# Kernel tuning notes

Hardware: AMD Instinct MI355X
Metric: run time of the kernel (lower is better)

The kernel has to match this reference:

```python
import jax, jax.numpy as jnp
import numpy as np

H, W, D = 200, 200, 16          # voxel grid dims
GRID = 0.4                       # voxel size (m)
MULT = 3.0                       # scale_multiplier (3-sigma radius)
PC_MIN = np.array([-40.0, -40.0, -1.0], dtype=np.float32)
B, N, M, C = 1, 16384, 4096, 18  # batch, query points, gaussians, semantic classes


def setup_inputs() -> dict:
    key = jax.random.key(0)
    ks = jax.random.split(key, 6)
    extent = jnp.array([H, W, D], dtype=jnp.float32) * GRID
    pc_min = jnp.asarray(PC_MIN)
    # points / means strictly inside the grid so int-voxel asserts hold
    pts = pc_min + jax.random.uniform(ks[0], (B, N, 3), dtype=jnp.float32) * (extent - 1e-3)
    means3D = pc_min + jax.random.uniform(ks[1], (B, M, 3), dtype=jnp.float32) * (extent - 1e-3)
    opacities = jax.random.uniform(ks[2], (B, M), dtype=jnp.float32, minval=0.1, maxval=1.0)
    semantics = jax.random.normal(ks[3], (B, M, C), dtype=jnp.float32)
    # scales chosen so ceil(max_scale*3/0.4) >= 1 (radii assert)
    scales = jax.random.uniform(ks[4], (B, M, 3), dtype=jnp.float32, minval=0.15, maxval=0.6)
    # SPD covariance per Gaussian: diag(scales^2) + small PSD perturbation
    Bm = 0.05 * jax.random.normal(ks[5], (B, M, 3, 3), dtype=jnp.float32)
    cov3D = jnp.eye(3, dtype=jnp.float32) * (scales ** 2)[..., :, None] + Bm @ jnp.swapaxes(Bm, -1, -2)
    return {"pts": pts, "means3D": means3D, "opacities": opacities,
            "semantics": semantics, "scales": scales, "cov3D": cov3D}


def _aggregate(pts_i, means_i, op_i, sem_i, sc_i, cov_i):
    # pts_i [N,3], means_i [M,3], op_i [M], sem_i [M,C], sc_i [M,3], cov_i [M,3,3]
    pc_min = jnp.asarray(PC_MIN)
    pint = jnp.floor((pts_i - pc_min) / GRID).astype(jnp.int32)    # [N,3] voxel of each point
    mint = jnp.floor((means_i - pc_min) / GRID).astype(jnp.int32)  # [M,3] voxel of each gaussian
    radii = jnp.ceil(jnp.max(sc_i, axis=-1) * MULT / GRID).astype(jnp.int32)  # [M] voxel radius
    A = jnp.linalg.inv(cov_i)                                       # [M,3,3] conic (inverse cov)
    Am = jnp.einsum('gij,gj->gi', A, means_i)                       # [M,3]
    mAm = jnp.einsum('gi,gi->g', means_i, Am)                       # [M]
    # Mahalanobis q[n,g] = (p-m)^T A (p-m) = p^T A p - 2 p^T A m + m^T A m, via [N,9]x[9,M] GEMM
    pp = (pts_i[:, :, None] * pts_i[:, None, :]).reshape(-1, 9)     # [N,9]
    pAp = pp @ A.reshape(-1, 9).T                                   # [N,M]
    q = pAp - 2.0 * (pts_i @ Am.T) + mAm[None, :]                   # [N,M]
    # gaussian contributes to a point iff the point's voxel lies in the gaussian's radius box
    mask = jnp.all(jnp.abs(pint[:, None, :] - mint[None, :, :]) <= radii[None, :, None], axis=-1)
    w = jnp.where(mask, jnp.exp(-0.5 * q) * op_i[None, :], 0.0)     # [N,M]
    return w @ sem_i                                                # [N,C] logits


def reference(pts, means3D, opacities, semantics, scales, cov3D):
    return jax.vmap(_aggregate)(pts, means3D, opacities, semantics, scales, cov3D)
```

## Files before the change

### kernel.cpp

```cpp
#include <hip/hip_runtime.h>

namespace {
constexpr float GRIDSZ = 0.4f;
constexpr float PCX = -40.0f, PCY = -40.0f, PCZ = -1.0f;
constexpr int CCH = 18;
constexpr int CELLS_X = 25;
constexpr int NCELLS = CELLS_X * CELLS_X;
constexpr int VMAX = 199;
constexpr int PCAP = 128;
constexpr int GCAP = 128;
constexpr int SEMW = 20;
}

__global__ __launch_bounds__(256) void prep_kernel(
    const float* __restrict__ pts, const float* __restrict__ means,
    const float* __restrict__ opac, const float* __restrict__ scales,
    const float* __restrict__ cov,
    unsigned* __restrict__ ppack, float4* __restrict__ ppos,
    unsigned* __restrict__ gcb, int4* __restrict__ gbox,
    float4* __restrict__ gpay, int N, int M) {
  int id = blockIdx.x * 256 + threadIdx.x;
  if (id < M) {
    int g = id;
    float mx = means[(size_t)g * 3 + 0], my = means[(size_t)g * 3 + 1], mz = means[(size_t)g * 3 + 2];
    const float* c = cov + (size_t)g * 9;
    float c00 = c[0], c01 = c[1], c02 = c[2], c11 = c[4], c12 = c[5], c22 = c[8];
    float M00 = c11 * c22 - c12 * c12;
    float M01 = c02 * c12 - c01 * c22;
    float M02 = c01 * c12 - c02 * c11;
    float inv = 1.0f / (c00 * M00 + c01 * M01 + c02 * M02);
    int mvx = (int)floorf((mx - PCX) / GRIDSZ);
    int mvy = (int)floorf((my - PCY) / GRIDSZ);
    int mvz = (int)floorf((mz - PCZ) / GRIDSZ);
    float smax = fmaxf(scales[(size_t)g * 3 + 0],
                 fmaxf(scales[(size_t)g * 3 + 1], scales[(size_t)g * 3 + 2]));
    int r = (int)ceilf(smax * 3.0f / GRIDSZ);
    gbox[g] = make_int4(mvx - r, mvy - r, mvz - r, 2 * r);
    int cx0 = max(mvx - r, 0) >> 3, cx1 = min(mvx + r, VMAX) >> 3;
    int cy0 = max(mvy - r, 0) >> 3, cy1 = min(mvy + r, VMAX) >> 3;
    gcb[g] = (unsigned)cx0 | ((unsigned)cx1 << 8) | ((unsigned)cy0 << 16) | ((unsigned)cy1 << 24);
    gpay[(size_t)g * 3 + 0] = make_float4(mx, my, mz, opac[g]);
    gpay[(size_t)g * 3 + 1] = make_float4(M00 * inv, M01 * inv, M02 * inv,
                                          (c00 * c22 - c02 * c02) * inv);
    gpay[(size_t)g * 3 + 2] = make_float4((c01 * c02 - c00 * c12) * inv,
                                          (c00 * c11 - c01 * c01) * inv, 0.f, 0.f);
  } else if (id < M + N) {
    int p = id - M;
    float px = pts[(size_t)p * 3 + 0], py = pts[(size_t)p * 3 + 1], pz = pts[(size_t)p * 3 + 2];
    int pvx = (int)floorf((px - PCX) / GRIDSZ);
    int pvy = (int)floorf((py - PCY) / GRIDSZ);
    int pvz = (int)floorf((pz - PCZ) / GRIDSZ);
    unsigned cell = (unsigned)((pvx >> 3) + CELLS_X * (pvy >> 3));
    ppack[p] = cell | ((unsigned)pvx << 10) | ((unsigned)pvy << 18) | ((unsigned)pvz << 26);
    ppos[p] = make_float4(px, py, pz, __int_as_float(p));
  }
}

__global__ __launch_bounds__(256) void agg_kernel(
    const unsigned* __restrict__ ppack, const float4* __restrict__ ppos,
    const unsigned* __restrict__ gcb, const int4* __restrict__ gbox,
    const float4* __restrict__ gpay, const float* __restrict__ sem,
    float* __restrict__ out, int N, int M) {
  __shared__ int pcnt_s, gcnt_s;
  __shared__ unsigned lvox[PCAP];
  __shared__ int lpi[PCAP];
  __shared__ float4 lpts[PCAP];
  __shared__ int graw[GCAP];
  __shared__ int gsrt[GCAP];
  __shared__ int4 lbox[GCAP];
  __shared__ float4 lpay[GCAP * 3];
  __shared__ float lsem[GCAP * SEMW];
  __shared__ float buf[3][64][CCH + 1];

  const int tid = threadIdx.x, lane = tid & 63, wave = tid >> 6;
  const unsigned cell = blockIdx.x;
  const int cx = (int)(cell % CELLS_X), cy = (int)(cell / CELLS_X);

  if (tid == 0) { pcnt_s = 0; gcnt_s = 0; }
  __syncthreads();

  {
    const uint4* pp4 = reinterpret_cast<const uint4*>(ppack);
    const int n4 = N >> 2;
    for (int i4 = tid; i4 < n4; i4 += 256) {
      uint4 v = pp4[i4];
      unsigned pk[4] = {v.x, v.y, v.z, v.w};
#pragma unroll
      for (int k = 0; k < 4; ++k) {
        if ((pk[k] & 1023u) == cell) {
          int s = atomicAdd(&pcnt_s, 1);
          if (s < PCAP) { lvox[s] = pk[k]; lpi[s] = i4 * 4 + k; }
        }
      }
    }
    for (int i = (n4 << 2) + tid; i < N; i += 256) {
      unsigned pk = ppack[i];
      if ((pk & 1023u) == cell) {
        int s = atomicAdd(&pcnt_s, 1);
        if (s < PCAP) { lvox[s] = pk; lpi[s] = i; }
      }
    }
  }
  {
    const uint4* gb4 = reinterpret_cast<const uint4*>(gcb);
    const int m4 = M >> 2;
    for (int i4 = tid; i4 < m4; i4 += 256) {
      uint4 v = gb4[i4];
      unsigned gk[4] = {v.x, v.y, v.z, v.w};
#pragma unroll
      for (int k = 0; k < 4; ++k) {
        unsigned pk = gk[k];
        bool hit = (cx >= (int)(pk & 255u)) & (cx <= (int)((pk >> 8) & 255u)) &
                   (cy >= (int)((pk >> 16) & 255u)) & (cy <= (int)(pk >> 24));
        if (hit) {
          int s = atomicAdd(&gcnt_s, 1);
          if (s < GCAP) graw[s] = i4 * 4 + k;
        }
      }
    }
    for (int g = (m4 << 2) + tid; g < M; g += 256) {
      unsigned pk = gcb[g];
      bool hit = (cx >= (int)(pk & 255u)) & (cx <= (int)((pk >> 8) & 255u)) &
                 (cy >= (int)((pk >> 16) & 255u)) & (cy <= (int)(pk >> 24));
      if (hit) {
        int s = atomicAdd(&gcnt_s, 1);
        if (s < GCAP) graw[s] = g;
      }
    }
  }
  __syncthreads();
  const int P = min(pcnt_s, PCAP);
  const int K = min(gcnt_s, GCAP);

  if (tid < K) {
    int v = graw[tid], rank = 0;
    for (int j = 0; j < K; ++j) rank += (graw[j] < v);
    gsrt[rank] = v;
  }
  __syncthreads();

  if (tid < P) lpts[tid] = ppos[lpi[tid]];
  for (int j = tid; j < K; j += 256) lbox[j] = gbox[gsrt[j]];
  for (int idx = tid; idx < K * 3; idx += 256) {
    int j = idx / 3, k = idx - j * 3;
    lpay[idx] = gpay[(size_t)gsrt[j] * 3 + k];
  }
  for (int idx = tid; idx < K * CCH; idx += 256) {
    int j = idx / CCH, c2 = idx - j * CCH;
    lsem[j * SEMW + c2] = sem[(size_t)gsrt[j] * CCH + c2];
  }
  __syncthreads();

  const int kq = (K + 3) >> 2;
  const int j0 = wave * kq, j1 = min(K, j0 + kq);

  for (int pb = 0; pb < P; pb += 64) {
    const bool vp = (pb + lane) < P;
    const float4 pt = lpts[vp ? pb + lane : 0];
    const unsigned pk = vp ? lvox[pb + lane] : 0u;
    int pvx = (int)((pk >> 10) & 255u);
    int pvy = (int)((pk >> 18) & 255u);
    int pvz = (int)(pk >> 26);
    if (!vp) pvx = -100000;

    float acc[CCH];
#pragma unroll
    for (int c = 0; c < CCH; ++c) acc[c] = 0.f;

    for (int j = j0; j < j1; ++j) {
      int4 bx = lbox[j];
      bool m = ((unsigned)(pvx - bx.x) <= (unsigned)bx.w) &
               ((unsigned)(pvy - bx.y) <= (unsigned)bx.w) &
               ((unsigned)(pvz - bx.z) <= (unsigned)bx.w);
      if (__any(m)) {
        float4 q0 = lpay[j * 3 + 0];
        float4 q1 = lpay[j * 3 + 1];
        float4 q2 = lpay[j * 3 + 2];
        float dx = pt.x - q0.x, dy = pt.y - q0.y, dz = pt.z - q0.z;
        float t0 = q1.x * dx + q1.y * dy + q1.z * dz;
        float t1 = q1.y * dx + q1.w * dy + q2.x * dz;
        float t2 = q1.z * dx + q2.x * dy + q2.y * dz;
        float qq = dx * t0 + dy * t1 + dz * t2;
        float w = m ? __expf(-0.5f * qq) * q0.w : 0.f;
        const float4* s4 = reinterpret_cast<const float4*>(&lsem[j * SEMW]);
        float4 sa = s4[0], sb = s4[1], sc = s4[2], sd = s4[3];
        float2 se = *reinterpret_cast<const float2*>(&lsem[j * SEMW + 16]);
        acc[0]  = fmaf(w, sa.x, acc[0]);  acc[1]  = fmaf(w, sa.y, acc[1]);
        acc[2]  = fmaf(w, sa.z, acc[2]);  acc[3]  = fmaf(w, sa.w, acc[3]);
        acc[4]  = fmaf(w, sb.x, acc[4]);  acc[5]  = fmaf(w, sb.y, acc[5]);
        acc[6]  = fmaf(w, sb.z, acc[6]);  acc[7]  = fmaf(w, sb.w, acc[7]);
        acc[8]  = fmaf(w, sc.x, acc[8]);  acc[9]  = fmaf(w, sc.y, acc[9]);
        acc[10] = fmaf(w, sc.z, acc[10]); acc[11] = fmaf(w, sc.w, acc[11]);
        acc[12] = fmaf(w, sd.x, acc[12]); acc[13] = fmaf(w, sd.y, acc[13]);
        acc[14] = fmaf(w, sd.z, acc[14]); acc[15] = fmaf(w, sd.w, acc[15]);
        acc[16] = fmaf(w, se.x, acc[16]); acc[17] = fmaf(w, se.y, acc[17]);
      }
    }

    if (wave > 0) {
#pragma unroll
      for (int c = 0; c < CCH; ++c) buf[wave - 1][lane][c] = acc[c];
    }
    __syncthreads();
    if (wave == 0 && vp) {
      int myp = __float_as_int(pt.w);
      float* o = out + (size_t)myp * CCH;
#pragma unroll
      for (int c = 0; c < CCH; ++c)
        o[c] = acc[c] + buf[0][lane][c] + buf[1][lane][c] + buf[2][lane][c];
    }
    __syncthreads();
  }
}

extern "C" void kernel_launch(void* const* d_in, const int* in_sizes, int n_in,
                              void* d_out, int out_size, void* d_ws, size_t ws_size,
                              hipStream_t stream) {
  const float* pts     = (const float*)d_in[0];
  const float* means3D = (const float*)d_in[1];
  const float* opac    = (const float*)d_in[2];
  const float* sem     = (const float*)d_in[3];
  const float* scales  = (const float*)d_in[4];
  const float* cov3D   = (const float*)d_in[5];
  float* out = (float*)d_out;

  int N = in_sizes[0] / 3;
  int M = in_sizes[1] / 3;

  char* ws = (char*)d_ws;
  size_t off = 0;
  auto alloc = [&](size_t bytes) { char* p = ws + off; off = (off + bytes + 255) & ~(size_t)255; return p; };
  unsigned* ppack = (unsigned*)alloc((size_t)N * 4);
  float4*   ppos  = (float4*)alloc((size_t)N * 16);
  unsigned* gcb   = (unsigned*)alloc((size_t)M * 4);
  int4*     gbox  = (int4*)alloc((size_t)M * 16);
  float4*   gpay  = (float4*)alloc((size_t)M * 48);

  prep_kernel<<<(N + M + 255) / 256, 256, 0, stream>>>(
      pts, means3D, opac, scales, cov3D, ppack, ppos, gcb, gbox, gpay, N, M);

  agg_kernel<<<NCELLS, 256, 0, stream>>>(
      ppack, ppos, gcb, gbox, gpay, sem, out, N, M);
}
```

Measured before the change: 26.15 us.

## Shrink prep output to 16-bit cell ids and compute gaussian payloads in agg

The prep kernel now writes only a 16-bit cell index per point and the cell-bounds word per gaussian, dropping the intermediate position, box and inverse-covariance buffers. The aggregation kernel rebuilds point voxels and gaussian boxes and conics from the raw inputs, but only for the points and gaussians that fall in its cell. The per-cell point scan reads half as many bytes. In exchange, the conic inversion is repeated in every cell a gaussian overlaps, and the agg kernel now does gathers from the strided raw arrays.

```diff
diff --git a/kernel.cpp b/kernel.cpp
--- a/kernel.cpp
+++ b/kernel.cpp
@@ -2,7 +2,8 @@
 
 namespace {
 constexpr float GRIDSZ = 0.4f;
-constexpr float PCX = -40.0f, PCY = -40.0f, PCZ = -1.0f;
+constexpr float PCXY = -40.0f;
+constexpr float PCZ  = -1.0f;
 constexpr int CCH = 18;
 constexpr int CELLS_X = 25;
 constexpr int NCELLS = CELLS_X * CELLS_X;
@@ -14,56 +15,39 @@
 
 __global__ __launch_bounds__(256) void prep_kernel(
     const float* __restrict__ pts, const float* __restrict__ means,
-    const float* __restrict__ opac, const float* __restrict__ scales,
-    const float* __restrict__ cov,
-    unsigned* __restrict__ ppack, float4* __restrict__ ppos,
-    unsigned* __restrict__ gcb, int4* __restrict__ gbox,
-    float4* __restrict__ gpay, int N, int M) {
+    const float* __restrict__ scales,
+    unsigned short* __restrict__ pcell, unsigned* __restrict__ gcb,
+    int N, int M) {
   int id = blockIdx.x * 256 + threadIdx.x;
   if (id < M) {
     int g = id;
-    float mx = means[(size_t)g * 3 + 0], my = means[(size_t)g * 3 + 1], mz = means[(size_t)g * 3 + 2];
-    const float* c = cov + (size_t)g * 9;
-    float c00 = c[0], c01 = c[1], c02 = c[2], c11 = c[4], c12 = c[5], c22 = c[8];
-    float M00 = c11 * c22 - c12 * c12;
-    float M01 = c02 * c12 - c01 * c22;
-    float M02 = c01 * c12 - c02 * c11;
-    float inv = 1.0f / (c00 * M00 + c01 * M01 + c02 * M02);
-    int mvx = (int)floorf((mx - PCX) / GRIDSZ);
-    int mvy = (int)floorf((my - PCY) / GRIDSZ);
-    int mvz = (int)floorf((mz - PCZ) / GRIDSZ);
+    float mx = means[(size_t)g * 3 + 0], my = means[(size_t)g * 3 + 1];
+    int mvx = (int)floorf((mx - PCXY) / GRIDSZ);
+    int mvy = (int)floorf((my - PCXY) / GRIDSZ);
     float smax = fmaxf(scales[(size_t)g * 3 + 0],
                  fmaxf(scales[(size_t)g * 3 + 1], scales[(size_t)g * 3 + 2]));
     int r = (int)ceilf(smax * 3.0f / GRIDSZ);
-    gbox[g] = make_int4(mvx - r, mvy - r, mvz - r, 2 * r);
     int cx0 = max(mvx - r, 0) >> 3, cx1 = min(mvx + r, VMAX) >> 3;
     int cy0 = max(mvy - r, 0) >> 3, cy1 = min(mvy + r, VMAX) >> 3;
     gcb[g] = (unsigned)cx0 | ((unsigned)cx1 << 8) | ((unsigned)cy0 << 16) | ((unsigned)cy1 << 24);
-    gpay[(size_t)g * 3 + 0] = make_float4(mx, my, mz, opac[g]);
-    gpay[(size_t)g * 3 + 1] = make_float4(M00 * inv, M01 * inv, M02 * inv,
-                                          (c00 * c22 - c02 * c02) * inv);
-    gpay[(size_t)g * 3 + 2] = make_float4((c01 * c02 - c00 * c12) * inv,
-                                          (c00 * c11 - c01 * c01) * inv, 0.f, 0.f);
   } else if (id < M + N) {
     int p = id - M;
-    float px = pts[(size_t)p * 3 + 0], py = pts[(size_t)p * 3 + 1], pz = pts[(size_t)p * 3 + 2];
-    int pvx = (int)floorf((px - PCX) / GRIDSZ);
-    int pvy = (int)floorf((py - PCY) / GRIDSZ);
-    int pvz = (int)floorf((pz - PCZ) / GRIDSZ);
-    unsigned cell = (unsigned)((pvx >> 3) + CELLS_X * (pvy >> 3));
-    ppack[p] = cell | ((unsigned)pvx << 10) | ((unsigned)pvy << 18) | ((unsigned)pvz << 26);
-    ppos[p] = make_float4(px, py, pz, __int_as_float(p));
+    float px = pts[(size_t)p * 3 + 0], py = pts[(size_t)p * 3 + 1];
+    int pvx = (int)floorf((px - PCXY) / GRIDSZ);
+    int pvy = (int)floorf((py - PCXY) / GRIDSZ);
+    pcell[p] = (unsigned short)((pvx >> 3) + CELLS_X * (pvy >> 3));
   }
 }
 
 __global__ __launch_bounds__(256) void agg_kernel(
-    const unsigned* __restrict__ ppack, const float4* __restrict__ ppos,
-    const unsigned* __restrict__ gcb, const int4* __restrict__ gbox,
-    const float4* __restrict__ gpay, const float* __restrict__ sem,
+    const float* __restrict__ pts, const float* __restrict__ means,
+    const float* __restrict__ opac, const float* __restrict__ scales,
+    const float* __restrict__ cov, const float* __restrict__ sem,
+    const unsigned short* __restrict__ pcell, const unsigned* __restrict__ gcb,
     float* __restrict__ out, int N, int M) {
   __shared__ int pcnt_s, gcnt_s;
-  __shared__ unsigned lvox[PCAP];
   __shared__ int lpi[PCAP];
+  __shared__ int lvox[PCAP];
   __shared__ float4 lpts[PCAP];
   __shared__ int graw[GCAP];
   __shared__ int gsrt[GCAP];
@@ -73,31 +57,34 @@
   __shared__ float buf[3][64][CCH + 1];
 
   const int tid = threadIdx.x, lane = tid & 63, wave = tid >> 6;
-  const unsigned cell = blockIdx.x;
-  const int cx = (int)(cell % CELLS_X), cy = (int)(cell / CELLS_X);
+  const unsigned cellv = blockIdx.x;
+  const int cx = (int)(cellv % CELLS_X), cy = (int)(cellv / CELLS_X);
 
   if (tid == 0) { pcnt_s = 0; gcnt_s = 0; }
   __syncthreads();
 
   {
-    const uint4* pp4 = reinterpret_cast<const uint4*>(ppack);
-    const int n4 = N >> 2;
-    for (int i4 = tid; i4 < n4; i4 += 256) {
-      uint4 v = pp4[i4];
-      unsigned pk[4] = {v.x, v.y, v.z, v.w};
+    const uint4* pc4 = reinterpret_cast<const uint4*>(pcell);
+    const int n8 = N >> 3;
+    for (int i8 = tid; i8 < n8; i8 += 256) {
+      uint4 v = pc4[i8];
+      unsigned w[4] = {v.x, v.y, v.z, v.w};
 #pragma unroll
       for (int k = 0; k < 4; ++k) {
-        if ((pk[k] & 1023u) == cell) {
+        if ((w[k] & 0xFFFFu) == cellv) {
           int s = atomicAdd(&pcnt_s, 1);
-          if (s < PCAP) { lvox[s] = pk[k]; lpi[s] = i4 * 4 + k; }
+          if (s < PCAP) lpi[s] = i8 * 8 + 2 * k;
         }
-      }
-    }
-    for (int i = (n4 << 2) + tid; i < N; i += 256) {
-      unsigned pk = ppack[i];
-      if ((pk & 1023u) == cell) {
+        if ((w[k] >> 16) == cellv) {
+          int s = atomicAdd(&pcnt_s, 1);
+          if (s < PCAP) lpi[s] = i8 * 8 + 2 * k + 1;
+        }
+      }
+    }
+    for (int i = (n8 << 3) + tid; i < N; i += 256) {
+      if (pcell[i] == cellv) {
         int s = atomicAdd(&pcnt_s, 1);
-        if (s < PCAP) { lvox[s] = pk; lpi[s] = i; }
+        if (s < PCAP) lpi[s] = i;
       }
     }
   }
@@ -139,11 +126,36 @@
   }
   __syncthreads();
 
-  if (tid < P) lpts[tid] = ppos[lpi[tid]];
-  for (int j = tid; j < K; j += 256) lbox[j] = gbox[gsrt[j]];
-  for (int idx = tid; idx < K * 3; idx += 256) {
-    int j = idx / 3, k = idx - j * 3;
-    lpay[idx] = gpay[(size_t)gsrt[j] * 3 + k];
+  if (tid < P) {
+    int i = lpi[tid];
+    float px = pts[(size_t)i * 3], py = pts[(size_t)i * 3 + 1], pz = pts[(size_t)i * 3 + 2];
+    int pvx = (int)floorf((px - PCXY) / GRIDSZ);
+    int pvy = (int)floorf((py - PCXY) / GRIDSZ);
+    int pvz = (int)floorf((pz - PCZ) / GRIDSZ);
+    lvox[tid] = pvx | (pvy << 8) | (pvz << 16);
+    lpts[tid] = make_float4(px, py, pz, __int_as_float(i));
+  } else if (tid >= 128 && tid - 128 < K) {
+    int t = tid - 128;
+    int g = gsrt[t];
+    float mx = means[(size_t)g * 3], my = means[(size_t)g * 3 + 1], mz = means[(size_t)g * 3 + 2];
+    int mvx = (int)floorf((mx - PCXY) / GRIDSZ);
+    int mvy = (int)floorf((my - PCXY) / GRIDSZ);
+    int mvz = (int)floorf((mz - PCZ) / GRIDSZ);
+    float sm = fmaxf(scales[(size_t)g * 3],
+               fmaxf(scales[(size_t)g * 3 + 1], scales[(size_t)g * 3 + 2]));
+    int r = (int)ceilf(sm * 3.0f / GRIDSZ);
+    lbox[t] = make_int4(mvx - r, mvy - r, mvz - r, 2 * r);
+    const float* c = cov + (size_t)g * 9;
+    float c00 = c[0], c01 = c[1], c02 = c[2], c11 = c[4], c12 = c[5], c22 = c[8];
+    float M00 = c11 * c22 - c12 * c12;
+    float M01 = c02 * c12 - c01 * c22;
+    float M02 = c01 * c12 - c02 * c11;
+    float inv = 1.0f / (c00 * M00 + c01 * M01 + c02 * M02);
+    lpay[t * 3 + 0] = make_float4(mx, my, mz, opac[g]);
+    lpay[t * 3 + 1] = make_float4(M00 * inv, M01 * inv, M02 * inv,
+                                  (c00 * c22 - c02 * c02) * inv);
+    lpay[t * 3 + 2] = make_float4((c01 * c02 - c00 * c12) * inv,
+                                  (c00 * c11 - c01 * c01) * inv, 0.f, 0.f);
   }
   for (int idx = tid; idx < K * CCH; idx += 256) {
     int j = idx / CCH, c2 = idx - j * CCH;
@@ -157,11 +169,10 @@
   for (int pb = 0; pb < P; pb += 64) {
     const bool vp = (pb + lane) < P;
     const float4 pt = lpts[vp ? pb + lane : 0];
-    const unsigned pk = vp ? lvox[pb + lane] : 0u;
-    int pvx = (int)((pk >> 10) & 255u);
-    int pvy = (int)((pk >> 18) & 255u);
-    int pvz = (int)(pk >> 26);
-    if (!vp) pvx = -100000;
+    const int pv = vp ? lvox[pb + lane] : 0;
+    int pvx = vp ? (pv & 255) : -100000;
+    int pvy = (pv >> 8) & 255;
+    int pvz = pv >> 16;
 
     float acc[CCH];
 #pragma unroll
@@ -230,15 +241,12 @@
   char* ws = (char*)d_ws;
   size_t off = 0;
   auto alloc = [&](size_t bytes) { char* p = ws + off; off = (off + bytes + 255) & ~(size_t)255; return p; };
-  unsigned* ppack = (unsigned*)alloc((size_t)N * 4);
-  float4*   ppos  = (float4*)alloc((size_t)N * 16);
-  unsigned* gcb   = (unsigned*)alloc((size_t)M * 4);
-  int4*     gbox  = (int4*)alloc((size_t)M * 16);
-  float4*   gpay  = (float4*)alloc((size_t)M * 48);
+  unsigned short* pcell = (unsigned short*)alloc((size_t)N * 2);
+  unsigned*       gcb   = (unsigned*)alloc((size_t)M * 4);
 
   prep_kernel<<<(N + M + 255) / 256, 256, 0, stream>>>(
-      pts, means3D, opac, scales, cov3D, ppack, ppos, gcb, gbox, gpay, N, M);
+      pts, means3D, scales, pcell, gcb, N, M);
 
   agg_kernel<<<NCELLS, 256, 0, stream>>>(
-      ppack, ppos, gcb, gbox, gpay, sem, out, N, M);
-}
+      pts, means3D, opac, scales, cov3D, sem, pcell, gcb, out, N, M);
+}
```

Result: faster. 22.17 us (-15.3%).
